# Kernel optimization log

Measured on AMD Instinct MI355X. Metric: run time of the kernel, lower is better.

Reference implementation:

```python
import jax, jax.numpy as jnp
import numpy as np

N = 50000
E = 800000
IN, HID, OUT = 256, 128, 64
NEG_SLOPE = 0.2


def _gat(x, src, dst, W, a_src, a_dst, b, heads, dim, concat):
    # PyG GATConv (eval mode, self-loops already appended to src/dst)
    xh = (x @ W).reshape(N, heads, dim)              # [N,H,D]
    s_src = jnp.einsum('nhd,hd->nh', xh, a_src)       # [N,H]
    s_dst = jnp.einsum('nhd,hd->nh', xh, a_dst)
    e = jax.nn.leaky_relu(s_src[src] + s_dst[dst], NEG_SLOPE)  # [Etot,H]
    m = jax.ops.segment_max(e, dst, num_segments=N)
    e = jnp.exp(e - m[dst])
    z = jax.ops.segment_sum(e, dst, num_segments=N)
    alpha = e / z[dst]                                # segment softmax over incoming edges
    msg = xh[src] * alpha[:, :, None]                 # [Etot,H,D] gather + weight
    out = jax.ops.segment_sum(msg, dst, num_segments=N)  # scatter-add aggregate
    out = out.reshape(N, heads * dim) if concat else out.mean(axis=1)
    return out + b


def setup_inputs():
    key = jax.random.key(0)
    ks = jax.random.split(key, 20)
    sc = 0.05
    inp = {
        'x': jax.random.normal(ks[0], (N, IN), jnp.float32),
        'edge_index': jax.random.randint(ks[1], (2, E), 0, N, jnp.int64) if jax.config.read('jax_enable_x64') else jax.random.randint(ks[1], (2, E), 0, N, jnp.int32),
        # semantic MLP
        'w1': jax.random.normal(ks[2], (IN, HID), jnp.float32) * sc,
        'b1': jnp.zeros((HID,), jnp.float32),
        'w2': jax.random.normal(ks[3], (HID, HID), jnp.float32) * sc,
        'b2': jnp.zeros((HID,), jnp.float32),
        # gat1: HID -> HID//2, heads=4, concat -> 2*HID
        'g1_w': jax.random.normal(ks[4], (HID, 4 * (HID // 2)), jnp.float32) * sc,
        'g1_asrc': jax.random.normal(ks[5], (4, HID // 2), jnp.float32) * sc,
        'g1_adst': jax.random.normal(ks[6], (4, HID // 2), jnp.float32) * sc,
        'g1_b': jnp.zeros((2 * HID,), jnp.float32),
        # gat2: 2*HID -> OUT, heads=2, mean
        'g2_w': jax.random.normal(ks[7], (2 * HID, 2 * OUT), jnp.float32) * sc,
        'g2_asrc': jax.random.normal(ks[8], (2, OUT), jnp.float32) * sc,
        'g2_adst': jax.random.normal(ks[9], (2, OUT), jnp.float32) * sc,
        'g2_b': jnp.zeros((OUT,), jnp.float32),
        # gat3: OUT -> OUT, heads=1, mean
        'g3_w': jax.random.normal(ks[10], (OUT, OUT), jnp.float32) * sc,
        'g3_asrc': jax.random.normal(ks[11], (1, OUT), jnp.float32) * sc,
        'g3_adst': jax.random.normal(ks[12], (1, OUT), jnp.float32) * sc,
        'g3_b': jnp.zeros((OUT,), jnp.float32),
    }
    return inp


def reference(x, edge_index, w1, b1, w2, b2,
              g1_w, g1_asrc, g1_adst, g1_b,
              g2_w, g2_asrc, g2_adst, g2_b,
              g3_w, g3_asrc, g3_adst, g3_b):
    # add self loops once (PyG GATConv default add_self_loops=True)
    loop = jnp.arange(N, dtype=edge_index.dtype)
    src = jnp.concatenate([edge_index[0], loop])
    dst = jnp.concatenate([edge_index[1], loop])
    # semantic MLP (eval: dropout is identity)
    h = jax.nn.relu(x @ w1 + b1)
    h = jax.nn.relu(h @ w2 + b2)
    h = jax.nn.elu(_gat(h, src, dst, g1_w, g1_asrc, g1_adst, g1_b, 4, HID // 2, True))
    h = jax.nn.elu(_gat(h, src, dst, g2_w, g2_asrc, g2_adst, g2_b, 2, OUT, False))
    h = _gat(h, src, dst, g3_w, g3_asrc, g3_adst, g3_b, 1, OUT, False)
    return h
```

## Files before the change

### kernel.cpp

```cpp
#include <hip/hip_runtime.h>
#include <hip/hip_fp16.h>
#include <math.h>

#define NN 50000
#define NE 800000

static inline int ceil_div_h(int a, int b) { return (a + b - 1) / b; }

typedef _Float16 half8 __attribute__((ext_vector_type(8)));
typedef float f32x4 __attribute__((ext_vector_type(4)));

__global__ __launch_bounds__(256)
void prep_kernel(const float* __restrict__ w1, const float* __restrict__ w2,
                 const float* __restrict__ g1w, const float* __restrict__ g2w,
                 const float* __restrict__ g3w, __half* __restrict__ wt,
                 int* __restrict__ cursor) {
  int idx = blockIdx.x * 256 + threadIdx.x;
  if (idx < NN) cursor[idx] = 0;
  const float* W; int K, N, li;
  if (idx < 32768)        { W = w1;  K = 256; N = 128; li = idx; }
  else if (idx < 49152)   { W = w2;  K = 128; N = 128; li = idx - 32768; }
  else if (idx < 81920)   { W = g1w; K = 128; N = 256; li = idx - 49152; }
  else if (idx < 114688)  { W = g2w; K = 256; N = 128; li = idx - 81920; }
  else if (idx < 118784)  { W = g3w; K = 64;  N = 64;  li = idx - 114688; }
  else return;
  int n = li / K, k = li - n * K;
  wt[idx] = __float2half_rn(W[(size_t)k * N + n]);
}

__global__ __launch_bounds__(256)
void mlp_gat1_fused(const float* __restrict__ x,
                    const __half* __restrict__ wt1,
                    const float* __restrict__ b1,
                    const __half* __restrict__ wt2,
                    const float* __restrict__ b2,
                    const __half* __restrict__ wtg1,
                    const float* __restrict__ a_src, const float* __restrict__ a_dst,
                    __half* __restrict__ xh1,
                    float* __restrict__ s_src, float* __restrict__ s_dst) {
  constexpr int SA = 40;
  constexpr int SH = 136;
  __shared__ __align__(16) _Float16 smem[25088];
  _Float16* As   = smem;
  _Float16* Bs12 = smem + 2560;
  _Float16* h1s  = smem + 7680;
  _Float16* h2s  = smem + 16384;
  _Float16* Bs3  = Bs12;
  const int tid = threadIdx.x;
  const int bm = blockIdx.x * 64;
  const int wave = tid >> 6, lane = tid & 63;
  const int l16 = lane & 15, quad = lane >> 4;
  const int wm = (wave & 1) * 32;
  const int wn = (wave >> 1) * 64;

  {
    f32x4 acc[2][4] = {};
    for (int k0 = 0; k0 < 256; k0 += 32) {
      #pragma unroll
      for (int i = 0; i < 2; ++i) {
        int idx = tid + i * 256;
        int m = idx >> 3, q = idx & 7;
        int gm = bm + m;
        float4 v = make_float4(0.f, 0.f, 0.f, 0.f);
        if (gm < NN) v = *(const float4*)&x[(size_t)gm * 256 + k0 + q * 4];
        union { __half2 h2[2]; float2 f2; } u;
        u.h2[0] = __floats2half2_rn(v.x, v.y);
        u.h2[1] = __floats2half2_rn(v.z, v.w);
        *(float2*)&As[m * SA + q * 4] = u.f2;
      }
      #pragma unroll
      for (int i = 0; i < 2; ++i) {
        int idx = tid + i * 256;
        int n = idx >> 2, kq = (idx & 3) * 8;
        *(float4*)&Bs12[n * SA + kq] = *(const float4*)&wt1[(size_t)n * 256 + k0 + kq];
      }
      __syncthreads();
      half8 af[2], bf[4];
      #pragma unroll
      for (int mi = 0; mi < 2; ++mi)
        af[mi] = *(const half8*)&As[(wm + mi * 16 + l16) * SA + quad * 8];
      #pragma unroll
      for (int ni = 0; ni < 4; ++ni)
        bf[ni] = *(const half8*)&Bs12[(wn + ni * 16 + l16) * SA + quad * 8];
      #pragma unroll
      for (int mi = 0; mi < 2; ++mi)
        #pragma unroll
        for (int ni = 0; ni < 4; ++ni)
          acc[mi][ni] = __builtin_amdgcn_mfma_f32_16x16x32_f16(af[mi], bf[ni], acc[mi][ni], 0, 0, 0);
      __syncthreads();
    }
    #pragma unroll
    for (int mi = 0; mi < 2; ++mi)
      #pragma unroll
      for (int r = 0; r < 4; ++r) {
        int row = wm + mi * 16 + quad * 4 + r;
        #pragma unroll
        for (int ni = 0; ni < 4; ++ni) {
          int col = wn + ni * 16 + l16;
          float v = acc[mi][ni][r] + b1[col];
          v = fmaxf(v, 0.f);
          h1s[row * SH + col] = (_Float16)v;
        }
      }
  }
  __syncthreads();

  {
    f32x4 acc[2][4] = {};
    for (int k0 = 0; k0 < 128; k0 += 32) {
      #pragma unroll
      for (int i = 0; i < 2; ++i) {
        int idx = tid + i * 256;
        int n = idx >> 2, kq = (idx & 3) * 8;
        *(float4*)&Bs12[n * SA + kq] = *(const float4*)&wt2[(size_t)n * 128 + k0 + kq];
      }
      __syncthreads();
      half8 af[2], bf[4];
      #pragma unroll
      for (int mi = 0; mi < 2; ++mi)
        af[mi] = *(const half8*)&h1s[(wm + mi * 16 + l16) * SH + k0 + quad * 8];
      #pragma unroll
      for (int ni = 0; ni < 4; ++ni)
        bf[ni] = *(const half8*)&Bs12[(wn + ni * 16 + l16) * SA + quad * 8];
      #pragma unroll
      for (int mi = 0; mi < 2; ++mi)
        #pragma unroll
        for (int ni = 0; ni < 4; ++ni)
          acc[mi][ni] = __builtin_amdgcn_mfma_f32_16x16x32_f16(af[mi], bf[ni], acc[mi][ni], 0, 0, 0);
      __syncthreads();
    }
    #pragma unroll
    for (int mi = 0; mi < 2; ++mi)
      #pragma unroll
      for (int r = 0; r < 4; ++r) {
        int row = wm + mi * 16 + quad * 4 + r;
        #pragma unroll
        for (int ni = 0; ni < 4; ++ni) {
          int col = wn + ni * 16 + l16;
          float v = acc[mi][ni][r] + b2[col];
          v = fmaxf(v, 0.f);
          h2s[row * SH + col] = (_Float16)v;
        }
      }
  }
  __syncthreads();

  {
    f32x4 acc[4][4] = {};
    const int wn3 = wave * 64;
    for (int k0 = 0; k0 < 128; k0 += 32) {
      #pragma unroll
      for (int i = 0; i < 4; ++i) {
        int idx = tid + i * 256;
        int n = idx >> 2, kq = (idx & 3) * 8;
        *(float4*)&Bs3[n * SA + kq] = *(const float4*)&wtg1[(size_t)n * 128 + k0 + kq];
      }
      __syncthreads();
      half8 af[4], bf[4];
      #pragma unroll
      for (int mi = 0; mi < 4; ++mi)
        af[mi] = *(const half8*)&h2s[(mi * 16 + l16) * SH + k0 + quad * 8];
      #pragma unroll
      for (int ni = 0; ni < 4; ++ni)
        bf[ni] = *(const half8*)&Bs3[(wn3 + ni * 16 + l16) * SA + quad * 8];
      #pragma unroll
      for (int mi = 0; mi < 4; ++mi)
        #pragma unroll
        for (int ni = 0; ni < 4; ++ni)
          acc[mi][ni] = __builtin_amdgcn_mfma_f32_16x16x32_f16(af[mi], bf[ni], acc[mi][ni], 0, 0, 0);
      __syncthreads();
    }
    float asv[4], adv[4];
    #pragma unroll
    for (int ni = 0; ni < 4; ++ni) {
      int d = ni * 16 + l16;
      asv[ni] = a_src[wave * 64 + d];
      adv[ni] = a_dst[wave * 64 + d];
    }
    #pragma unroll
    for (int mi = 0; mi < 4; ++mi) {
      #pragma unroll
      for (int r = 0; r < 4; ++r) {
        int gm = bm + mi * 16 + quad * 4 + r;
        float ss = 0.f, sd = 0.f;
        #pragma unroll
        for (int ni = 0; ni < 4; ++ni) {
          float v = acc[mi][ni][r];
          ss = fmaf(v, asv[ni], ss);
          sd = fmaf(v, adv[ni], sd);
          if (gm < NN) xh1[(size_t)gm * 256 + wn3 + ni * 16 + l16] = __float2half_rn(v);
        }
        #pragma unroll
        for (int off = 1; off < 16; off <<= 1) {
          ss += __shfl_xor(ss, off, 64);
          sd += __shfl_xor(sd, off, 64);
        }
        if (l16 == 0 && gm < NN) {
          s_src[gm * 4 + wave] = ss;
          s_dst[gm * 4 + wave] = sd;
        }
      }
    }
  }
}

template<int BM, int TN, int WR, int WC, int ACT, int OUTH, int AF32, int HS>
__global__ __launch_bounds__(256)
void mfma_gemm(const void* __restrict__ Av, const __half* __restrict__ Bt,
               const float* __restrict__ bias, void* __restrict__ Cv,
               const float* __restrict__ a_src, const float* __restrict__ a_dst,
               float* __restrict__ s_src, float* __restrict__ s_dst,
               int M, int N, int K) {
  constexpr int FM = BM / WR / 16;
  constexpr int FN = TN / WC / 16;
  constexpr int SA = 40;
  __shared__ __align__(16) _Float16 As[BM * SA];
  __shared__ __align__(16) _Float16 Bs[TN * SA];
  const int tid = threadIdx.x;
  const int bm = blockIdx.y * BM, bn = blockIdx.x * TN;
  const int wave = tid >> 6, lane = tid & 63;
  const int wm = (wave % WR) * (BM / WR);
  const int wn = (wave / WR) * (TN / WC);
  const int l16 = lane & 15, quad = lane >> 4;

  f32x4 acc[FM][FN] = {};

  for (int k0 = 0; k0 < K; k0 += 32) {
    if (AF32) {
      const float* A = (const float*)Av;
      #pragma unroll
      for (int i = 0; i < (BM * 8) / 256; ++i) {
        int idx = tid + i * 256;
        int m = idx >> 3, q = idx & 7;
        int gm = bm + m;
        float4 v = make_float4(0.f, 0.f, 0.f, 0.f);
        if (gm < M) v = *(const float4*)&A[(size_t)gm * K + k0 + q * 4];
        union { __half2 h2[2]; float2 f2; } u;
        u.h2[0] = __floats2half2_rn(v.x, v.y);
        u.h2[1] = __floats2half2_rn(v.z, v.w);
        *(float2*)&As[m * SA + q * 4] = u.f2;
      }
    } else {
      const __half* A = (const __half*)Av;
      #pragma unroll
      for (int i = 0; i < (BM * 4) / 256; ++i) {
        int idx = tid + i * 256;
        int m = idx >> 2, q = (idx & 3) * 8;
        int gm = bm + m;
        float4 raw = make_float4(0.f, 0.f, 0.f, 0.f);
        if (gm < M) raw = *(const float4*)&A[(size_t)gm * K + k0 + q];
        *(float4*)&As[m * SA + q] = raw;
      }
    }
    #pragma unroll
    for (int i = 0; i < (TN * 4) / 256; ++i) {
      int idx = tid + i * 256;
      int n = idx >> 2, kq = (idx & 3) * 8;
      float4 raw = *(const float4*)&Bt[(size_t)(bn + n) * K + k0 + kq];
      *(float4*)&Bs[n * SA + kq] = raw;
    }
    __syncthreads();
    half8 af[FM], bf[FN];
    #pragma unroll
    for (int mi = 0; mi < FM; ++mi)
      af[mi] = *(const half8*)&As[(wm + mi * 16 + l16) * SA + quad * 8];
    #pragma unroll
    for (int ni = 0; ni < FN; ++ni)
      bf[ni] = *(const half8*)&Bs[(wn + ni * 16 + l16) * SA + quad * 8];
    #pragma unroll
    for (int mi = 0; mi < FM; ++mi)
      #pragma unroll
      for (int ni = 0; ni < FN; ++ni)
        acc[mi][ni] = __builtin_amdgcn_mfma_f32_16x16x32_f16(af[mi], bf[ni], acc[mi][ni], 0, 0, 0);
    __syncthreads();
  }

  #pragma unroll
  for (int mi = 0; mi < FM; ++mi) {
    #pragma unroll
    for (int r = 0; r < 4; ++r) {
      int gm = bm + wm + mi * 16 + quad * 4 + r;
      if (gm >= M) continue;
      #pragma unroll
      for (int ni = 0; ni < FN; ++ni) {
        int gn = bn + wn + ni * 16 + l16;
        float v = acc[mi][ni][r];
        if (bias) v += bias[gn];
        if (ACT == 1) v = fmaxf(v, 0.f);
        if (OUTH) ((__half*)Cv)[(size_t)gm * N + gn] = __float2half_rn(v);
        else      ((float*)Cv)[(size_t)gm * N + gn] = v;
      }
    }
  }

  if (HS > 0) {
    const int h = (bn + wn) >> 6;
    float asv[FN], adv[FN];
    #pragma unroll
    for (int ni = 0; ni < FN; ++ni) {
      int d = ni * 16 + l16;
      asv[ni] = a_src[h * 64 + d];
      adv[ni] = a_dst[h * 64 + d];
    }
    #pragma unroll
    for (int mi = 0; mi < FM; ++mi) {
      #pragma unroll
      for (int r = 0; r < 4; ++r) {
        float ss = 0.f, sd = 0.f;
        #pragma unroll
        for (int ni = 0; ni < FN; ++ni) {
          float v = acc[mi][ni][r];
          ss = fmaf(v, asv[ni], ss);
          sd = fmaf(v, adv[ni], sd);
        }
        #pragma unroll
        for (int off = 1; off < 16; off <<= 1) {
          ss += __shfl_xor(ss, off, 64);
          sd += __shfl_xor(sd, off, 64);
        }
        int gm = bm + wm + mi * 16 + quad * 4 + r;
        if (l16 == 0 && gm < M) {
          s_src[gm * HS + h] = ss;
          s_dst[gm * HS + h] = sd;
        }
      }
    }
  }
}


__global__ __launch_bounds__(256)
void hist_kernel(const int* __restrict__ ei, int* __restrict__ cnt) {
  int e = blockIdx.x * blockDim.x + threadIdx.x;
  if (e >= NE) return;
  atomicAdd(&cnt[ei[NE + e]], 1);
}

__global__ __launch_bounds__(256)
void scan1_kernel(const int* __restrict__ in, int* __restrict__ out,
                  int* __restrict__ bsum, int n) {
  __shared__ int tmp[256];
  int t = threadIdx.x;
  int i = blockIdx.x * 256 + t;
  int v = (i < n) ? in[i] : 0;
  tmp[t] = v;
  __syncthreads();
  for (int off = 1; off < 256; off <<= 1) {
    int u = (t >= off) ? tmp[t - off] : 0;
    __syncthreads();
    tmp[t] += u;
    __syncthreads();
  }
  if (i <= n) out[i] = tmp[t] - v;
  if (t == 255) bsum[blockIdx.x] = tmp[255];
}

__global__ __launch_bounds__(256)
void scan3_kernel(int* __restrict__ out, const int* __restrict__ bsum,
                  int* __restrict__ cursor, int n, int nb) {
  __shared__ int tmp[256];
  int t = threadIdx.x;
  int bv = (t < nb) ? bsum[t] : 0;
  tmp[t] = bv;
  __syncthreads();
  for (int off = 1; off < 256; off <<= 1) {
    int u = (t >= off) ? tmp[t - off] : 0;
    __syncthreads();
    tmp[t] += u;
    __syncthreads();
  }
  int add = tmp[blockIdx.x] - ((blockIdx.x < nb) ? bsum[blockIdx.x] : 0);
  int i = blockIdx.x * 256 + t;
  if (i > n) return;
  int v = out[i] + add;
  out[i] = v;
  if (i < n) cursor[i] = v;
}

__global__ __launch_bounds__(256)
void scatter_kernel(const int* __restrict__ ei, int* __restrict__ cursor,
                    int* __restrict__ srcs) {
  int e = blockIdx.x * blockDim.x + threadIdx.x;
  if (e >= NE) return;
  int s = ei[e], d = ei[NE + e];
  int pos = atomicAdd(&cursor[d], 1);
  srcs[pos] = s;
}

__global__ __launch_bounds__(256)
void gat_aggregate4(const int* __restrict__ rowptr, const int* __restrict__ srcs,
                    const float* __restrict__ ssrc, const float* __restrict__ sdst,
                    const __half* __restrict__ xh, const float* __restrict__ bias,
                    __half* __restrict__ out) {
  constexpr int H = 4, HD = 256;
  __shared__ float wbuf[4][64 * H];
  __shared__ int sbuf[4][64];
  const int wslot = threadIdx.x >> 6;
  const int wid = (blockIdx.x * blockDim.x + threadIdx.x) >> 6;
  const int lane = threadIdx.x & 63;
  if (wid >= NN) return;
  const int n = wid;
  const int start = rowptr[n];
  const int end = rowptr[n + 1];
  const int h = lane >> 4;

  float sdv[H];
  #pragma unroll
  for (int hh = 0; hh < H; ++hh) sdv[hh] = sdst[n * H + hh];

  float z;
  float acc[H];
  {
    float wself[H];
    #pragma unroll
    for (int hh = 0; hh < H; ++hh) {
      float e = ssrc[n * H + hh] + sdv[hh];
      e = e >= 0.f ? e : 0.2f * e;
      wself[hh] = __expf(e);
    }
    float ws = wself[h];
    z = ws;
    const __half* xr = xh + (size_t)n * HD + lane * H;
    float2 raw = *(const float2*)xr;
    __half2 p0 = *(__half2*)&raw.x;
    __half2 p1 = *(__half2*)&raw.y;
    float2 f0 = __half22float2(p0), f1 = __half22float2(p1);
    acc[0] = ws * f0.x; acc[1] = ws * f0.y; acc[2] = ws * f1.x; acc[3] = ws * f1.y;
  }

  for (int base = start; base < end; base += 64) {
    int cnt = end - base;
    if (cnt > 64) cnt = 64;
    if (lane < cnt) {
      int s = srcs[base + lane];
      sbuf[wslot][lane] = s;
      float4 t = *(const float4*)&ssrc[s * 4];
      float ev[H] = {t.x, t.y, t.z, t.w};
      #pragma unroll
      for (int hh = 0; hh < H; ++hh) {
        float e = ev[hh] + sdv[hh];
        e = e >= 0.f ? e : 0.2f * e;
        wbuf[wslot][lane * H + hh] = __expf(e);
      }
    }
    #pragma unroll 4
    for (int j = 0; j < cnt; ++j) {
      int s = sbuf[wslot][j];
      float w = wbuf[wslot][j * H + h];
      z += w;
      const __half* xr = xh + (size_t)s * HD + lane * H;
      float2 raw = *(const float2*)xr;
      __half2 p0 = *(__half2*)&raw.x;
      __half2 p1 = *(__half2*)&raw.y;
      float2 f0 = __half22float2(p0), f1 = __half22float2(p1);
      acc[0] = fmaf(w, f0.x, acc[0]); acc[1] = fmaf(w, f0.y, acc[1]);
      acc[2] = fmaf(w, f1.x, acc[2]); acc[3] = fmaf(w, f1.y, acc[3]);
    }
  }
  const float inv = 1.f / z;

  float v[4];
  #pragma unroll
  for (int i = 0; i < 4; ++i) {
    v[i] = acc[i] * inv + bias[lane * 4 + i];
    v[i] = v[i] > 0.f ? v[i] : expm1f(v[i]);
  }
  union { __half2 h2[2]; float2 f2; } u;
  u.h2[0] = __floats2half2_rn(v[0], v[1]);
  u.h2[1] = __floats2half2_rn(v[2], v[3]);
  *(float2*)&out[(size_t)n * 256 + lane * 4] = u.f2;
}

template<int H, int MODE>
__global__ __launch_bounds__(256)
void gat_aggregate_ms(const int* __restrict__ rowptr, const int* __restrict__ srcs,
                      const float* __restrict__ ssrc, const float* __restrict__ sdst,
                      const __half* __restrict__ xh, const float* __restrict__ bias,
                      void* __restrict__ outv) {
  constexpr int HD   = H * 64;
  constexpr int L8   = HD / 4;
  constexpr int NSUB = 64 / L8;
  __shared__ float wbuf[4][64 * H];
  __shared__ int sbuf[4][64];
  const int wslot = threadIdx.x >> 6;
  const int wid = (blockIdx.x * blockDim.x + threadIdx.x) >> 6;
  const int lane = threadIdx.x & 63;
  if (wid >= NN) return;
  const int n = wid;
  const int start = rowptr[n];
  const int end = rowptr[n + 1];
  const int sub = lane / L8;
  const int p = lane - sub * L8;
  const int hp = (p * 4) >> 6;

  float sdv[H];
  #pragma unroll
  for (int hh = 0; hh < H; ++hh) sdv[hh] = sdst[n * H + hh];

  float z = 0.f;
  float a0 = 0.f, a1 = 0.f, a2 = 0.f, a3 = 0.f;
  {
    float e = ssrc[n * H + hp] + sdv[hp];
    e = e >= 0.f ? e : 0.2f * e;
    float ws = __expf(e);
    if (sub == 0) {
      z = ws;
      float2 raw = *(const float2*)(xh + (size_t)n * HD + p * 4);
      __half2 q0 = *(__half2*)&raw.x, q1 = *(__half2*)&raw.y;
      float2 f0 = __half22float2(q0), f1 = __half22float2(q1);
      a0 = ws * f0.x; a1 = ws * f0.y; a2 = ws * f1.x; a3 = ws * f1.y;
    }
  }

  for (int base = start; base < end; base += 64) {
    int cnt = end - base;
    if (cnt > 64) cnt = 64;
    int cnt_pad = (cnt + NSUB - 1) & ~(NSUB - 1);
    if (lane < cnt) {
      int s = srcs[base + lane];
      sbuf[wslot][lane] = s;
      float ev[H];
      if (H == 2) {
        float2 t = *(const float2*)&ssrc[s * 2];
        ev[0] = t.x; ev[1] = t.y;
      } else {
        ev[0] = ssrc[s];
      }
      #pragma unroll
      for (int hh = 0; hh < H; ++hh) {
        float e = ev[hh] + sdv[hh];
        e = e >= 0.f ? e : 0.2f * e;
        wbuf[wslot][lane * H + hh] = __expf(e);
      }
    } else if (lane < cnt_pad) {
      sbuf[wslot][lane] = n;
      #pragma unroll
      for (int hh = 0; hh < H; ++hh) wbuf[wslot][lane * H + hh] = 0.f;
    }
    #pragma unroll 4
    for (int j = 0; j < cnt; j += NSUB) {
      int e = j + sub;
      int s = sbuf[wslot][e];
      float w = wbuf[wslot][e * H + hp];
      z += w;
      float2 raw = *(const float2*)(xh + (size_t)s * HD + p * 4);
      __half2 q0 = *(__half2*)&raw.x, q1 = *(__half2*)&raw.y;
      float2 f0 = __half22float2(q0), f1 = __half22float2(q1);
      a0 = fmaf(w, f0.x, a0); a1 = fmaf(w, f0.y, a1);
      a2 = fmaf(w, f1.x, a2); a3 = fmaf(w, f1.y, a3);
    }
  }

  #pragma unroll
  for (int m = L8; m < 64; m <<= 1) {
    z += __shfl_xor(z, m, 64);
    a0 += __shfl_xor(a0, m, 64);
    a1 += __shfl_xor(a1, m, 64);
    a2 += __shfl_xor(a2, m, 64);
    a3 += __shfl_xor(a3, m, 64);
  }
  const float inv = 1.f / z;

  if (MODE == 1) {
    float v0 = a0 * inv, v1 = a1 * inv, v2 = a2 * inv, v3 = a3 * inv;
    float o0 = __shfl_xor(v0, 16, 64);
    float o1 = __shfl_xor(v1, 16, 64);
    float o2 = __shfl_xor(v2, 16, 64);
    float o3 = __shfl_xor(v3, 16, 64);
    if (sub == 0 && hp == 0) {
      float m0 = (v0 + o0) * 0.5f + bias[p * 4 + 0];
      float m1 = (v1 + o1) * 0.5f + bias[p * 4 + 1];
      float m2 = (v2 + o2) * 0.5f + bias[p * 4 + 2];
      float m3 = (v3 + o3) * 0.5f + bias[p * 4 + 3];
      m0 = m0 > 0.f ? m0 : expm1f(m0);
      m1 = m1 > 0.f ? m1 : expm1f(m1);
      m2 = m2 > 0.f ? m2 : expm1f(m2);
      m3 = m3 > 0.f ? m3 : expm1f(m3);
      __half* out = (__half*)outv;
      union { __half2 h2[2]; float2 f2; } u;
      u.h2[0] = __floats2half2_rn(m0, m1);
      u.h2[1] = __floats2half2_rn(m2, m3);
      *(float2*)&out[(size_t)n * 64 + p * 4] = u.f2;
    }
  } else {
    if (sub == 0) {
      float* out = (float*)outv;
      float4 o = make_float4(a0 * inv + bias[p * 4 + 0],
                             a1 * inv + bias[p * 4 + 1],
                             a2 * inv + bias[p * 4 + 2],
                             a3 * inv + bias[p * 4 + 3]);
      *(float4*)&out[(size_t)n * 64 + p * 4] = o;
    }
  }
}


extern "C" void kernel_launch(void* const* d_in, const int* in_sizes, int n_in,
                              void* d_out, int out_size, void* d_ws, size_t ws_size,
                              hipStream_t stream) {
  const float* x    = (const float*)d_in[0];
  const int*   ei   = (const int*)d_in[1];
  const float* w1   = (const float*)d_in[2];
  const float* b1   = (const float*)d_in[3];
  const float* w2   = (const float*)d_in[4];
  const float* b2   = (const float*)d_in[5];
  const float* g1w  = (const float*)d_in[6];
  const float* g1as = (const float*)d_in[7];
  const float* g1ad = (const float*)d_in[8];
  const float* g1b  = (const float*)d_in[9];
  const float* g2w  = (const float*)d_in[10];
  const float* g2as = (const float*)d_in[11];
  const float* g2ad = (const float*)d_in[12];
  const float* g2b  = (const float*)d_in[13];
  const float* g3w  = (const float*)d_in[14];
  const float* g3as = (const float*)d_in[15];
  const float* g3ad = (const float*)d_in[16];
  const float* g3b  = (const float*)d_in[17];
  float* out = (float*)d_out;

  float* ws   = (float*)d_ws;
  float* bufA = ws;
  float* bufB = bufA + (size_t)NN * 256;
  float* bufC = bufB + (size_t)NN * 256;
  float* ssrc = bufC + (size_t)NN * 256;
  float* sdst = ssrc + (size_t)NN * 4;
  int* rowptr = (int*)(sdst + (size_t)NN * 4);
  int* cursor = rowptr + (NN + 1);
  int* bsum   = cursor + NN;
  int* srcs   = bsum + 256;
  __half* wt   = (__half*)(srcs + NE);
  __half* wt1  = wt;
  __half* wt2  = wt + 32768;
  __half* wtg1 = wt + 49152;
  __half* wtg2 = wt + 81920;
  __half* wtg3 = wt + 114688;

  __half* xh1 = (__half*)bufC;
  __half* a1  = (__half*)bufA;
  __half* xh2 = (__half*)bufB;
  __half* a2  = (__half*)bufC;
  __half* xh3 = (__half*)bufB;

  const int TB = 256;
  const int grid_m = ceil_div_h(NN, 64);
  const int egrid = ceil_div_h(NE, TB);
  const int sgrid = ceil_div_h(NN + 1, TB);
  const int wgrid = ceil_div_h(NN, 4);

  prep_kernel<<<ceil_div_h(118784, TB), TB, 0, stream>>>(w1, w2, g1w, g2w, g3w, wt, cursor);

  hist_kernel<<<egrid, TB, 0, stream>>>(ei, cursor);
  scan1_kernel<<<sgrid, TB, 0, stream>>>(cursor, rowptr, bsum, NN);
  scan3_kernel<<<sgrid, TB, 0, stream>>>(rowptr, bsum, cursor, NN, sgrid);
  scatter_kernel<<<egrid, TB, 0, stream>>>(ei, cursor, srcs);

  mlp_gat1_fused<<<grid_m, TB, 0, stream>>>(x, wt1, b1, wt2, b2, wtg1,
                                            g1as, g1ad, xh1, ssrc, sdst);
  gat_aggregate4<<<wgrid, TB, 0, stream>>>(rowptr, srcs, ssrc, sdst, xh1, g1b, a1);

  mfma_gemm<64, 128, 2, 2, 0, 1, 0, 2><<<dim3(1, grid_m), TB, 0, stream>>>(
      a1, wtg2, nullptr, xh2, g2as, g2ad, ssrc, sdst, NN, 128, 256);
  gat_aggregate_ms<2, 1><<<wgrid, TB, 0, stream>>>(
      rowptr, srcs, ssrc, sdst, xh2, g2b, a2);

  mfma_gemm<64, 64, 4, 1, 0, 1, 0, 1><<<dim3(1, grid_m), TB, 0, stream>>>(
      a2, wtg3, nullptr, xh3, g3as, g3ad, ssrc, sdst, NN, 64, 64);
  gat_aggregate_ms<1, 2><<<wgrid, TB, 0, stream>>>(
      rowptr, srcs, ssrc, sdst, xh3, g3b, out);
}
```

Measured before the change: 396.5 us.

## Fuse GAT3 linear projection into GAT2 aggregation and drop scatter atomics

The GAT2 aggregation kernel now computes the 64x64 GAT3 projection and its attention scores per node, with one wavefront per node reading the fp16 weight row from global memory. This removes the separate MFMA GEMM launch and the round trip of the intermediate activations through memory. CSR construction also changes: the histogram atomic's return value is saved as a per-edge slot, so the scatter no longer needs a second atomic pass or a cursor array. In exchange, every node reloads the 8 KB g3 weight matrix, and the CSR edge order within each destination is still nondeterministic.

Measured after the change: 391.6 us. No clear change (-1.2%).

```diff
diff --git a/kernel.cpp b/kernel.cpp
--- a/kernel.cpp
+++ b/kernel.cpp
@@ -330,10 +330,11 @@
 
 
 __global__ __launch_bounds__(256)
-void hist_kernel(const int* __restrict__ ei, int* __restrict__ cnt) {
+void hist_kernel(const int* __restrict__ ei, int* __restrict__ cnt,
+                 int* __restrict__ eslot) {
   int e = blockIdx.x * blockDim.x + threadIdx.x;
   if (e >= NE) return;
-  atomicAdd(&cnt[ei[NE + e]], 1);
+  eslot[e] = atomicAdd(&cnt[ei[NE + e]], 1);
 }
 
 __global__ __launch_bounds__(256)
@@ -357,7 +358,7 @@
 
 __global__ __launch_bounds__(256)
 void scan3_kernel(int* __restrict__ out, const int* __restrict__ bsum,
-                  int* __restrict__ cursor, int n, int nb) {
+                  int n, int nb) {
   __shared__ int tmp[256];
   int t = threadIdx.x;
   int bv = (t < nb) ? bsum[t] : 0;
@@ -372,19 +373,16 @@
   int add = tmp[blockIdx.x] - ((blockIdx.x < nb) ? bsum[blockIdx.x] : 0);
   int i = blockIdx.x * 256 + t;
   if (i > n) return;
-  int v = out[i] + add;
-  out[i] = v;
-  if (i < n) cursor[i] = v;
-}
-
-__global__ __launch_bounds__(256)
-void scatter_kernel(const int* __restrict__ ei, int* __restrict__ cursor,
-                    int* __restrict__ srcs) {
+  out[i] = out[i] + add;
+}
+
+__global__ __launch_bounds__(256)
+void scatter_kernel(const int* __restrict__ ei, const int* __restrict__ rowptr,
+                    const int* __restrict__ eslot, int* __restrict__ srcs) {
   int e = blockIdx.x * blockDim.x + threadIdx.x;
   if (e >= NE) return;
   int s = ei[e], d = ei[NE + e];
-  int pos = atomicAdd(&cursor[d], 1);
-  srcs[pos] = s;
+  srcs[rowptr[d] + eslot[e]] = s;
 }
 
 __global__ __launch_bounds__(256)
@@ -471,17 +469,19 @@
   *(float2*)&out[(size_t)n * 256 + lane * 4] = u.f2;
 }
 
-template<int H, int MODE>
-__global__ __launch_bounds__(256)
-void gat_aggregate_ms(const int* __restrict__ rowptr, const int* __restrict__ srcs,
+__global__ __launch_bounds__(256)
+void gat_agg2_g3fused(const int* __restrict__ rowptr, const int* __restrict__ srcs,
                       const float* __restrict__ ssrc, const float* __restrict__ sdst,
-                      const __half* __restrict__ xh, const float* __restrict__ bias,
-                      void* __restrict__ outv) {
-  constexpr int HD   = H * 64;
-  constexpr int L8   = HD / 4;
-  constexpr int NSUB = 64 / L8;
+                      const __half* __restrict__ xh,
+                      const float* __restrict__ bias,
+                      const __half* __restrict__ wtg3,
+                      const float* __restrict__ a3s, const float* __restrict__ a3d,
+                      __half* __restrict__ xh3,
+                      float* __restrict__ s3src, float* __restrict__ s3dst) {
+  constexpr int H = 2, HD = 128, L8 = 32, NSUB = 2;
   __shared__ float wbuf[4][64 * H];
   __shared__ int sbuf[4][64];
+  __shared__ __align__(16) __half a2h[4][64];
   const int wslot = threadIdx.x >> 6;
   const int wid = (blockIdx.x * blockDim.x + threadIdx.x) >> 6;
   const int lane = threadIdx.x & 63;
@@ -519,13 +519,8 @@
     if (lane < cnt) {
       int s = srcs[base + lane];
       sbuf[wslot][lane] = s;
-      float ev[H];
-      if (H == 2) {
-        float2 t = *(const float2*)&ssrc[s * 2];
-        ev[0] = t.x; ev[1] = t.y;
-      } else {
-        ev[0] = ssrc[s];
-      }
+      float2 t = *(const float2*)&ssrc[s * 2];
+      float ev[H] = {t.x, t.y};
       #pragma unroll
       for (int hh = 0; hh < H; ++hh) {
         float e = ev[hh] + sdv[hh];
@@ -551,6 +546,131 @@
     }
   }
 
+  {
+    z += __shfl_xor(z, 32, 64);
+    a0 += __shfl_xor(a0, 32, 64);
+    a1 += __shfl_xor(a1, 32, 64);
+    a2 += __shfl_xor(a2, 32, 64);
+    a3 += __shfl_xor(a3, 32, 64);
+  }
+  const float inv = 1.f / z;
+
+  float v0 = a0 * inv, v1 = a1 * inv, v2 = a2 * inv, v3 = a3 * inv;
+  float o0 = __shfl_xor(v0, 16, 64);
+  float o1 = __shfl_xor(v1, 16, 64);
+  float o2 = __shfl_xor(v2, 16, 64);
+  float o3 = __shfl_xor(v3, 16, 64);
+  if (lane < 16) {
+    float m0 = (v0 + o0) * 0.5f + bias[lane * 4 + 0];
+    float m1 = (v1 + o1) * 0.5f + bias[lane * 4 + 1];
+    float m2 = (v2 + o2) * 0.5f + bias[lane * 4 + 2];
+    float m3 = (v3 + o3) * 0.5f + bias[lane * 4 + 3];
+    m0 = m0 > 0.f ? m0 : expm1f(m0);
+    m1 = m1 > 0.f ? m1 : expm1f(m1);
+    m2 = m2 > 0.f ? m2 : expm1f(m2);
+    m3 = m3 > 0.f ? m3 : expm1f(m3);
+    *(__half2*)&a2h[wslot][lane * 4]     = __floats2half2_rn(m0, m1);
+    *(__half2*)&a2h[wslot][lane * 4 + 2] = __floats2half2_rn(m2, m3);
+  }
+  __threadfence_block();
+
+  float acc3 = 0.f;
+  {
+    const float4* arow = (const float4*)&a2h[wslot][0];
+    const float4* wrow = (const float4*)(wtg3 + (size_t)lane * 64);
+    #pragma unroll
+    for (int i = 0; i < 8; ++i) {
+      float4 av = arow[i];
+      float4 wv = wrow[i];
+      const __half2* ah = (const __half2*)&av;
+      const __half2* wh = (const __half2*)&wv;
+      #pragma unroll
+      for (int j = 0; j < 4; ++j) {
+        float2 af = __half22float2(ah[j]);
+        float2 wf = __half22float2(wh[j]);
+        acc3 = fmaf(af.x, wf.x, acc3);
+        acc3 = fmaf(af.y, wf.y, acc3);
+      }
+    }
+  }
+  float s3s = acc3 * a3s[lane];
+  float s3d = acc3 * a3d[lane];
+  #pragma unroll
+  for (int off = 1; off < 64; off <<= 1) {
+    s3s += __shfl_xor(s3s, off, 64);
+    s3d += __shfl_xor(s3d, off, 64);
+  }
+  if (lane == 0) {
+    s3src[n] = s3s;
+    s3dst[n] = s3d;
+  }
+  xh3[(size_t)n * 64 + lane] = __float2half_rn(acc3);
+}
+
+__global__ __launch_bounds__(256)
+void gat_aggregate3(const int* __restrict__ rowptr, const int* __restrict__ srcs,
+                    const float* __restrict__ ssrc, const float* __restrict__ sdst,
+                    const __half* __restrict__ xh,
+                    const float* __restrict__ bias,
+                    float* __restrict__ out) {
+  constexpr int HD = 64, L8 = 16, NSUB = 4;
+  __shared__ float wbuf[4][64];
+  __shared__ int sbuf[4][64];
+  const int wslot = threadIdx.x >> 6;
+  const int wid = (blockIdx.x * blockDim.x + threadIdx.x) >> 6;
+  const int lane = threadIdx.x & 63;
+  if (wid >= NN) return;
+  const int n = wid;
+  const int start = rowptr[n];
+  const int end = rowptr[n + 1];
+  const int sub = lane / L8;
+  const int p = lane - sub * L8;
+
+  const float sdv = sdst[n];
+
+  float z = 0.f;
+  float a0 = 0.f, a1 = 0.f, a2 = 0.f, a3 = 0.f;
+  {
+    float e = ssrc[n] + sdv;
+    e = e >= 0.f ? e : 0.2f * e;
+    float ws = __expf(e);
+    if (sub == 0) {
+      z = ws;
+      float2 raw = *(const float2*)(xh + (size_t)n * HD + p * 4);
+      __half2 q0 = *(__half2*)&raw.x, q1 = *(__half2*)&raw.y;
+      float2 f0 = __half22float2(q0), f1 = __half22float2(q1);
+      a0 = ws * f0.x; a1 = ws * f0.y; a2 = ws * f1.x; a3 = ws * f1.y;
+    }
+  }
+
+  for (int base = start; base < end; base += 64) {
+    int cnt = end - base;
+    if (cnt > 64) cnt = 64;
+    int cnt_pad = (cnt + NSUB - 1) & ~(NSUB - 1);
+    if (lane < cnt) {
+      int s = srcs[base + lane];
+      sbuf[wslot][lane] = s;
+      float e = ssrc[s] + sdv;
+      e = e >= 0.f ? e : 0.2f * e;
+      wbuf[wslot][lane] = __expf(e);
+    } else if (lane < cnt_pad) {
+      sbuf[wslot][lane] = n;
+      wbuf[wslot][lane] = 0.f;
+    }
+    #pragma unroll 4
+    for (int j = 0; j < cnt; j += NSUB) {
+      int e = j + sub;
+      int s = sbuf[wslot][e];
+      float w = wbuf[wslot][e];
+      z += w;
+      float2 raw = *(const float2*)(xh + (size_t)s * HD + p * 4);
+      __half2 q0 = *(__half2*)&raw.x, q1 = *(__half2*)&raw.y;
+      float2 f0 = __half22float2(q0), f1 = __half22float2(q1);
+      a0 = fmaf(w, f0.x, a0); a1 = fmaf(w, f0.y, a1);
+      a2 = fmaf(w, f1.x, a2); a3 = fmaf(w, f1.y, a3);
+    }
+  }
+
   #pragma unroll
   for (int m = L8; m < 64; m <<= 1) {
     z += __shfl_xor(z, m, 64);
@@ -561,36 +681,12 @@
   }
   const float inv = 1.f / z;
 
-  if (MODE == 1) {
-    float v0 = a0 * inv, v1 = a1 * inv, v2 = a2 * inv, v3 = a3 * inv;
-    float o0 = __shfl_xor(v0, 16, 64);
-    float o1 = __shfl_xor(v1, 16, 64);
-    float o2 = __shfl_xor(v2, 16, 64);
-    float o3 = __shfl_xor(v3, 16, 64);
-    if (sub == 0 && hp == 0) {
-      float m0 = (v0 + o0) * 0.5f + bias[p * 4 + 0];
-      float m1 = (v1 + o1) * 0.5f + bias[p * 4 + 1];
-      float m2 = (v2 + o2) * 0.5f + bias[p * 4 + 2];
-      float m3 = (v3 + o3) * 0.5f + bias[p * 4 + 3];
-      m0 = m0 > 0.f ? m0 : expm1f(m0);
-      m1 = m1 > 0.f ? m1 : expm1f(m1);
-      m2 = m2 > 0.f ? m2 : expm1f(m2);
-      m3 = m3 > 0.f ? m3 : expm1f(m3);
-      __half* out = (__half*)outv;
-      union { __half2 h2[2]; float2 f2; } u;
-      u.h2[0] = __floats2half2_rn(m0, m1);
-      u.h2[1] = __floats2half2_rn(m2, m3);
-      *(float2*)&out[(size_t)n * 64 + p * 4] = u.f2;
-    }
-  } else {
-    if (sub == 0) {
-      float* out = (float*)outv;
-      float4 o = make_float4(a0 * inv + bias[p * 4 + 0],
-                             a1 * inv + bias[p * 4 + 1],
-                             a2 * inv + bias[p * 4 + 2],
-                             a3 * inv + bias[p * 4 + 3]);
-      *(float4*)&out[(size_t)n * 64 + p * 4] = o;
-    }
+  if (sub == 0) {
+    float4 o = make_float4(a0 * inv + bias[p * 4 + 0],
+                           a1 * inv + bias[p * 4 + 1],
+                           a2 * inv + bias[p * 4 + 2],
+                           a3 * inv + bias[p * 4 + 3]);
+    *(float4*)&out[(size_t)n * 64 + p * 4] = o;
   }
 }
 
@@ -638,8 +734,10 @@
   __half* xh1 = (__half*)bufC;
   __half* a1  = (__half*)bufA;
   __half* xh2 = (__half*)bufB;
-  __half* a2  = (__half*)bufC;
-  __half* xh3 = (__half*)bufB;
+  __half* xh3 = (__half*)bufA;
+  int* eslot  = (int*)bufB;
+  float* s3src = ssrc + 2 * NN;
+  float* s3dst = sdst + 2 * NN;
 
   const int TB = 256;
   const int grid_m = ceil_div_h(NN, 64);
@@ -649,10 +747,10 @@
 
   prep_kernel<<<ceil_div_h(118784, TB), TB, 0, stream>>>(w1, w2, g1w, g2w, g3w, wt, cursor);
 
-  hist_kernel<<<egrid, TB, 0, stream>>>(ei, cursor);
+  hist_kernel<<<egrid, TB, 0, stream>>>(ei, cursor, eslot);
   scan1_kernel<<<sgrid, TB, 0, stream>>>(cursor, rowptr, bsum, NN);
-  scan3_kernel<<<sgrid, TB, 0, stream>>>(rowptr, bsum, cursor, NN, sgrid);
-  scatter_kernel<<<egrid, TB, 0, stream>>>(ei, cursor, srcs);
+  scan3_kernel<<<sgrid, TB, 0, stream>>>(rowptr, bsum, NN, sgrid);
+  scatter_kernel<<<egrid, TB, 0, stream>>>(ei, rowptr, eslot, srcs);
 
   mlp_gat1_fused<<<grid_m, TB, 0, stream>>>(x, wt1, b1, wt2, b2, wtg1,
                                             g1as, g1ad, xh1, ssrc, sdst);
@@ -660,11 +758,10 @@
 
   mfma_gemm<64, 128, 2, 2, 0, 1, 0, 2><<<dim3(1, grid_m), TB, 0, stream>>>(
       a1, wtg2, nullptr, xh2, g2as, g2ad, ssrc, sdst, NN, 128, 256);
-  gat_aggregate_ms<2, 1><<<wgrid, TB, 0, stream>>>(
-      rowptr, srcs, ssrc, sdst, xh2, g2b, a2);
-
-  mfma_gemm<64, 64, 4, 1, 0, 1, 0, 1><<<dim3(1, grid_m), TB, 0, stream>>>(
-      a2, wtg3, nullptr, xh3, g3as, g3ad, ssrc, sdst, NN, 64, 64);
-  gat_aggregate_ms<1, 2><<<wgrid, TB, 0, stream>>>(
-      rowptr, srcs, ssrc, sdst, xh3, g3b, out);
-}
+
+  gat_agg2_g3fused<<<wgrid, TB, 0, stream>>>(
+      rowptr, srcs, ssrc, sdst, xh2, g2b, wtg3, g3as, g3ad, xh3, s3src, s3dst);
+
+  gat_aggregate3<<<wgrid, TB, 0, stream>>>(
+      rowptr, srcs, s3src, s3dst, xh3, g3b, out);
+}
```
